# Optimization experiments

Measured on AMD Instinct MI355X. Metric: run time of the kernel, lower is better.

Reference implementation:

```python
import jax, jax.numpy as jnp
import numpy as np

OUT_FEATURES = 16384
IN_FEATURES = 4096


def setup_inputs() -> dict:
    key = jax.random.key(0)
    k1, k2, k3, k4 = jax.random.split(key, 4)
    # activations [B, S, in]
    x = jax.random.normal(k1, (4, 2048, IN_FEATURES), dtype=jnp.float32)
    # packed int4 weights: two nibbles per uint8, total out*in values (even, no pad)
    n_packed = OUT_FEATURES * IN_FEATURES // 2
    weight_packed = jax.random.randint(k2, (n_packed,), 0, 256, dtype=jnp.int32).astype(jnp.uint8)
    # per-row dequant scale [out, 1], positive like abs-max/7
    scale = jax.random.uniform(k3, (OUT_FEATURES, 1), dtype=jnp.float32, minval=1e-3, maxval=0.05)
    bias = jax.random.normal(k4, (OUT_FEATURES,), dtype=jnp.float32) * 0.01
    return {"x": x, "weight_packed": weight_packed, "scale": scale, "bias": bias}


def reference(x, weight_packed, scale, bias):
    # unpack: even positions = low nibble, odd positions = high nibble
    low = (weight_packed & 15).astype(jnp.int8)
    high = ((weight_packed >> 4) & 15).astype(jnp.int8)
    q = jnp.stack([low, high], axis=-1).reshape(-1)  # interleave -> [out*in]
    # sign-extend 4-bit two's complement: values >7 map to negative
    q = jnp.where(q > 7, q - 16, q)
    # dequantize with per-row scale -> [out, in]
    w = q.reshape(OUT_FEATURES, IN_FEATURES).astype(jnp.float32) * scale
    # F.linear: y = x @ w.T + bias
    return jnp.einsum('bsi,oi->bso', x, w) + bias
```

## Files before the change

### kernel.cpp

```cpp
#include <hip/hip_runtime.h>
#include <hip/hip_bf16.h>
#include <stdint.h>

typedef short short8 __attribute__((ext_vector_type(8)));
typedef float floatx4 __attribute__((ext_vector_type(4)));

static constexpr int KTOT = 4096;
static constexpr int NTOT = 16384;
static constexpr int MTOT = 8192;

#define GLOAD_LDS16(g, l)                                              \
  __builtin_amdgcn_global_load_lds(                                    \
      (const __attribute__((address_space(1))) void*)(g),              \
      (__attribute__((address_space(3))) void*)(l), 16, 0, 0)

__device__ __forceinline__ uint32_t pack2_bf16_rne(float lo, float hi) {
  uint32_t a = __builtin_bit_cast(uint32_t, lo);
  uint32_t b = __builtin_bit_cast(uint32_t, hi);
  a += 0x7FFFu + ((a >> 16) & 1u);
  b += 0x7FFFu + ((b >> 16) & 1u);
  return __builtin_amdgcn_perm(b, a, 0x07060302u);
}


__global__ __launch_bounds__(256) void cvt_x_kernel(
    const float* __restrict__ X, ushort* __restrict__ Xb) {
  const size_t i = (size_t)blockIdx.x * 256 + threadIdx.x;
  const float4 a = *reinterpret_cast<const float4*>(X + i * 8);
  const float4 b = *reinterpret_cast<const float4*>(X + i * 8 + 4);
  uint4 o;
  o.x = pack2_bf16_rne(a.x, a.y);
  o.y = pack2_bf16_rne(a.z, a.w);
  o.z = pack2_bf16_rne(b.x, b.y);
  o.w = pack2_bf16_rne(b.z, b.w);
  *reinterpret_cast<uint4*>(Xb + i * 8) = o;
}

__global__ __launch_bounds__(256) void cvt_w_kernel(
    const uint32_t* __restrict__ Wp, ushort* __restrict__ Wb) {
  const size_t i = (size_t)blockIdx.x * 256 + threadIdx.x;
  const uint4 w = *reinterpret_cast<const uint4*>(Wp + i * 4);
  const uint32_t wd[4] = {w.x, w.y, w.z, w.w};
  uint4 o;
  uint32_t* op = reinterpret_cast<uint32_t*>(&o);
  #pragma unroll
  for (int p = 0; p < 4; ++p) {
    int v0 = ((int)(wd[p] << 28)) >> 28;
    int v1 = ((int)(wd[p] << 24)) >> 28;
    uint32_t f0 = __builtin_bit_cast(uint32_t, (float)v0);
    uint32_t f1 = __builtin_bit_cast(uint32_t, (float)v1);
    op[p] = __builtin_amdgcn_perm(f1, f0, 0x07060302u);
  }
  *reinterpret_cast<uint4*>(Wb + i * 8) = o;
}


static constexpr int BM = 256, BN = 256, BK = 32;
static constexpr int NT = KTOT / BK;

__global__ __launch_bounds__(512, 2) void gemm_bf16_256_kernel(
    const ushort* __restrict__ Xb,
    const ushort* __restrict__ Wb,
    const float* __restrict__ scale,
    const float* __restrict__ bias,
    float* __restrict__ Y)
{
  __shared__ ushort As[4 * 8192];
  __shared__ ushort Bs[4 * 8192];

  const int t    = threadIdx.x;
  const int lane = t & 63;
  const int wv   = t >> 6;
  const int wr   = wv >> 2;
  const int wcn  = wv & 3;

  const int wg  = blockIdx.x;
  const int xcd = wg & 7;
  const int s   = wg >> 3;
  const int bm0 = (xcd * 4 + (s & 3)) * BM;
  const int bn0 = (s >> 2) * BN;

  const int srow = wv * 16 + (lane >> 2);
  const int scol = 8 * ((lane & 3) ^ ((lane >> 2) & 3) ^ (lane >> 4));
  const ushort* agA = Xb + (size_t)(bm0 + srow) * KTOT + scol;
  const ushort* agB = Wb + (size_t)(bn0 + srow) * KTOT + scol;
  const size_t rowstep = (size_t)128 * KTOT;
  ushort* aldsw = As + wv * 512;
  ushort* bldsw = Bs + wv * 512;

  const int rcol = 8 * ((lane >> 4) ^ (lane & 3) ^ ((lane >> 2) & 3));
  const ushort* Abase = As + (wr * 128 + (lane & 15)) * 32 + rcol;
  const ushort* Bbase = Bs + (wcn * 64 + (lane & 15)) * 32 + rcol;

  floatx4 acc[8][4];
  #pragma unroll
  for (int m = 0; m < 8; ++m)
    #pragma unroll
    for (int n = 0; n < 4; ++n)
      acc[m][n] = (floatx4){0.f, 0.f, 0.f, 0.f};

  #pragma unroll
  for (int pt = 0; pt < 3; ++pt) {
    const size_t kof = (size_t)pt * BK;
    GLOAD_LDS16(agA + kof,           aldsw + pt * 8192);
    GLOAD_LDS16(agA + kof + rowstep, aldsw + pt * 8192 + 4096);
    GLOAD_LDS16(agB + kof,           bldsw + pt * 8192);
    GLOAD_LDS16(agB + kof + rowstep, bldsw + pt * 8192 + 4096);
  }
  asm volatile("s_waitcnt vmcnt(8)\ns_barrier" ::: "memory");

  for (int kt = 0; kt < NT; ++kt) {
    const int c  = kt & 3;
    const ushort* Ab = Abase + c * 8192;
    const ushort* Bb = Bbase + c * 8192;
    const int st = kt + 3;
    const bool do_stage = (st < NT);
    const int sb = st & 3;
    const size_t kof = (size_t)st * BK;

    short8 bf[4], af0[4], af1[4];
    #pragma unroll
    for (int n = 0; n < 4; ++n)
      bf[n] = *reinterpret_cast<const short8*>(Bb + n * 512);
    #pragma unroll
    for (int m = 0; m < 4; ++m)
      af0[m] = *reinterpret_cast<const short8*>(Ab + m * 512);
    #pragma unroll
    for (int m = 0; m < 4; ++m)
      af1[m] = *reinterpret_cast<const short8*>(Ab + (m + 4) * 512);

    if (do_stage) {
      GLOAD_LDS16(agA + kof,           aldsw + sb * 8192);
      GLOAD_LDS16(agA + kof + rowstep, aldsw + sb * 8192 + 4096);
      GLOAD_LDS16(agB + kof,           bldsw + sb * 8192);
      GLOAD_LDS16(agB + kof + rowstep, bldsw + sb * 8192 + 4096);
    }

    __builtin_amdgcn_s_setprio(1);
    #pragma unroll
    for (int m = 0; m < 4; ++m)
      #pragma unroll
      for (int n = 0; n < 4; ++n)
        acc[m][n] = __builtin_amdgcn_mfma_f32_16x16x32_bf16(af0[m], bf[n], acc[m][n], 0, 0, 0);
    #pragma unroll
    for (int m = 0; m < 4; ++m)
      #pragma unroll
      for (int n = 0; n < 4; ++n)
        acc[m + 4][n] = __builtin_amdgcn_mfma_f32_16x16x32_bf16(af1[m], bf[n], acc[m + 4][n], 0, 0, 0);
    __builtin_amdgcn_s_setprio(0);

    if (kt + 1 < NT) {
      if (kt + 4 <= NT)      { asm volatile("s_waitcnt vmcnt(8)\ns_barrier" ::: "memory"); }
      else if (kt + 3 <= NT) { asm volatile("s_waitcnt vmcnt(4)\ns_barrier" ::: "memory"); }
      else                   { asm volatile("s_waitcnt vmcnt(0)\ns_barrier" ::: "memory"); }
    }
  }

  const int crow = (lane >> 4) * 4;
  const int ccol = lane & 15;
  #pragma unroll
  for (int n = 0; n < 4; ++n) {
    const int col  = bn0 + wcn * 64 + n * 16 + ccol;
    const float sc = scale[col];
    const float bz = bias[col];
    #pragma unroll
    for (int m = 0; m < 8; ++m) {
      const int row0 = bm0 + wr * 128 + m * 16 + crow;
      float* yp = Y + (size_t)row0 * NTOT + col;
      #pragma unroll
      for (int r = 0; r < 4; ++r)
        yp[(size_t)r * NTOT] = acc[m][n][r] * sc + bz;
    }
  }
}


static constexpr int FBM = 128, FBN = 128, FBK = 64;
static constexpr int LDSS = 72;
static constexpr int FNSTEP = KTOT / FBK;

__global__ __launch_bounds__(256) void int4_linear_fused_kernel(
    const float* __restrict__ X,
    const uint32_t* __restrict__ Wp,
    const float* __restrict__ scale,
    const float* __restrict__ bias,
    float* __restrict__ Y)
{
  __shared__ ushort As[FBM * LDSS];
  __shared__ ushort Bs[FBN * LDSS];

  const int t    = threadIdx.x;
  const int lane = t & 63;
  const int wv   = t >> 6;
  const int wr   = wv >> 1;
  const int wc   = wv & 1;
  const int bm0 = blockIdx.y * FBM;
  const int bn0 = blockIdx.x * FBN;
  const int srow = t >> 1;
  const int sh   = t & 1;

  const float*    ag = X  + (size_t)(bm0 + srow) * KTOT + sh * 32;
  const uint32_t* bg = Wp + (size_t)(bn0 + srow) * (KTOT / 2) + sh * 16;

  float4 areg[8];
  uint4  breg[4];
  #pragma unroll
  for (int j = 0; j < 8; ++j) areg[j] = *reinterpret_cast<const float4*>(ag + j * 4);
  #pragma unroll
  for (int j = 0; j < 4; ++j) breg[j] = *reinterpret_cast<const uint4*>(bg + j * 4);

  floatx4 acc[4][4];
  #pragma unroll
  for (int m = 0; m < 4; ++m)
    #pragma unroll
    for (int n = 0; n < 4; ++n)
      acc[m][n] = (floatx4){0.f, 0.f, 0.f, 0.f};

  ushort* adst = &As[srow * LDSS + sh * 32];
  ushort* bdst = &Bs[srow * LDSS + sh * 32];

  for (int ks = 0; ks < FNSTEP; ++ks) {
    {
      uint32_t ab[16];
      #pragma unroll
      for (int j = 0; j < 8; ++j) {
        uint32_t u0 = __builtin_bit_cast(uint32_t, areg[j].x) + 0x8000u;
        uint32_t u1 = __builtin_bit_cast(uint32_t, areg[j].y) + 0x8000u;
        uint32_t u2 = __builtin_bit_cast(uint32_t, areg[j].z) + 0x8000u;
        uint32_t u3 = __builtin_bit_cast(uint32_t, areg[j].w) + 0x8000u;
        ab[2*j]   = __builtin_amdgcn_perm(u1, u0, 0x07060302u);
        ab[2*j+1] = __builtin_amdgcn_perm(u3, u2, 0x07060302u);
      }
      uint32_t bb[16];
      #pragma unroll
      for (int j = 0; j < 4; ++j) {
        const uint32_t wq[4] = {breg[j].x, breg[j].y, breg[j].z, breg[j].w};
        #pragma unroll
        for (int p = 0; p < 4; ++p) {
          const uint32_t w = wq[p];
          int v0 = ((int)(w << 28)) >> 28;
          int v1 = ((int)(w << 24)) >> 28;
          uint32_t f0 = __builtin_bit_cast(uint32_t, (float)v0);
          uint32_t f1 = __builtin_bit_cast(uint32_t, (float)v1);
          bb[j*4 + p] = __builtin_amdgcn_perm(f1, f0, 0x07060302u);
        }
      }
      #pragma unroll
      for (int j = 0; j < 4; ++j) {
        *reinterpret_cast<uint4*>(adst + j * 8) = *reinterpret_cast<const uint4*>(&ab[j*4]);
        *reinterpret_cast<uint4*>(bdst + j * 8) = *reinterpret_cast<const uint4*>(&bb[j*4]);
      }
    }
    __syncthreads();

    if (ks + 1 < FNSTEP) {
      const float*    ap = ag + (ks + 1) * FBK;
      const uint32_t* bp = bg + (ks + 1) * (FBK / 2);
      #pragma unroll
      for (int j = 0; j < 8; ++j) areg[j] = *reinterpret_cast<const float4*>(ap + j * 4);
      #pragma unroll
      for (int j = 0; j < 4; ++j) breg[j] = *reinterpret_cast<const uint4*>(bp + j * 4);
    }

    #pragma unroll
    for (int kk = 0; kk < 2; ++kk) {
      const int ko = kk * 32 + (lane >> 4) * 8;
      short8 af[4], bf[4];
      #pragma unroll
      for (int m = 0; m < 4; ++m)
        af[m] = *reinterpret_cast<const short8*>(&As[(wr*64 + m*16 + (lane & 15)) * LDSS + ko]);
      #pragma unroll
      for (int n = 0; n < 4; ++n)
        bf[n] = *reinterpret_cast<const short8*>(&Bs[(wc*64 + n*16 + (lane & 15)) * LDSS + ko]);
      #pragma unroll
      for (int m = 0; m < 4; ++m)
        #pragma unroll
        for (int n = 0; n < 4; ++n)
          acc[m][n] = __builtin_amdgcn_mfma_f32_16x16x32_bf16(af[m], bf[n], acc[m][n], 0, 0, 0);
    }
    __syncthreads();
  }

  const int crow = (lane >> 4) * 4;
  const int ccol = lane & 15;
  #pragma unroll
  for (int n = 0; n < 4; ++n) {
    const int col  = bn0 + wc * 64 + n * 16 + ccol;
    const float s  = scale[col];
    const float bz = bias[col];
    #pragma unroll
    for (int m = 0; m < 4; ++m) {
      const int row0 = bm0 + wr * 64 + m * 16 + crow;
      float* yp = Y + (size_t)row0 * NTOT + col;
      #pragma unroll
      for (int r = 0; r < 4; ++r)
        yp[(size_t)r * NTOT] = acc[m][n][r] * s + bz;
    }
  }
}


extern "C" void kernel_launch(void* const* d_in, const int* in_sizes, int n_in,
                              void* d_out, int out_size, void* d_ws, size_t ws_size,
                              hipStream_t stream) {
  (void)in_sizes; (void)n_in; (void)out_size;
  const float*    X     = (const float*)d_in[0];
  const uint32_t* Wp    = (const uint32_t*)d_in[1];
  const float*    scale = (const float*)d_in[2];
  const float*    bias  = (const float*)d_in[3];
  float*          Y     = (float*)d_out;

  const size_t xb_bytes = (size_t)MTOT * KTOT * 2;
  const size_t wb_bytes = (size_t)NTOT * KTOT * 2;
  if (ws_size >= xb_bytes + wb_bytes) {
    ushort* Xb = (ushort*)d_ws;
    ushort* Wb = (ushort*)((char*)d_ws + xb_bytes);
    cvt_x_kernel<<<(MTOT * KTOT) / (8 * 256), 256, 0, stream>>>(X, Xb);
    cvt_w_kernel<<<(NTOT * KTOT / 2) / (4 * 256), 256, 0, stream>>>(Wp, Wb);
    gemm_bf16_256_kernel<<<(MTOT / BM) * (NTOT / BN), 512, 0, stream>>>(Xb, Wb, scale, bias, Y);
  } else {
    dim3 grid(NTOT / FBN, MTOT / FBM);
    int4_linear_fused_kernel<<<grid, 256, 0, stream>>>(X, Wp, scale, bias, Y);
  }
}
```

Baseline: 1.182 ms.

## Double-buffer LDS fragments in registers across a 2x unrolled K loop

Unrolls the main K loop by two and keeps two register sets of A/B fragments. The fragments for the next k-tile are read from LDS before the MFMA cluster of the current tile runs, so LDS read latency overlaps matrix math. Wait counts and staging are adjusted so two tiles are resident before compute starts, and the barrier is shifted accordingly. This roughly doubles fragment register usage, which could pressure VGPRs under the 2-blocks-per-CU launch bound.

```diff
diff --git a/kernel.cpp b/kernel.cpp
--- a/kernel.cpp
+++ b/kernel.cpp
@@ -58,6 +58,49 @@
 static constexpr int BM = 256, BN = 256, BK = 32;
 static constexpr int NT = KTOT / BK;
 
+#define READ_FRAGS(AF0, AF1, BF, buf)                                   \
+  {                                                                     \
+    const ushort* Ab_ = Abase + (buf) * 8192;                           \
+    const ushort* Bb_ = Bbase + (buf) * 8192;                           \
+    _Pragma("unroll")                                                   \
+    for (int n = 0; n < 4; ++n)                                         \
+      BF[n] = *reinterpret_cast<const short8*>(Bb_ + n * 512);          \
+    _Pragma("unroll")                                                   \
+    for (int m = 0; m < 4; ++m)                                         \
+      AF0[m] = *reinterpret_cast<const short8*>(Ab_ + m * 512);         \
+    _Pragma("unroll")                                                   \
+    for (int m = 0; m < 4; ++m)                                         \
+      AF1[m] = *reinterpret_cast<const short8*>(Ab_ + (m + 4) * 512);   \
+  }
+
+#define STAGE(st_)                                                      \
+  if ((st_) < NT) {                                                     \
+    const int sb_ = (st_) & 3;                                          \
+    const size_t kof_ = (size_t)(st_) * BK;                             \
+    GLOAD_LDS16(agA + kof_,           aldsw + sb_ * 8192);              \
+    GLOAD_LDS16(agA + kof_ + rowstep, aldsw + sb_ * 8192 + 4096);      \
+    GLOAD_LDS16(agB + kof_,           bldsw + sb_ * 8192);              \
+    GLOAD_LDS16(agB + kof_ + rowstep, bldsw + sb_ * 8192 + 4096);      \
+  }
+
+#define MFMA_CLUSTER(AF0, AF1, BF)                                      \
+  __builtin_amdgcn_s_setprio(1);                                       \
+  _Pragma("unroll")                                                     \
+  for (int m = 0; m < 4; ++m)                                           \
+    _Pragma("unroll")                                                   \
+    for (int n = 0; n < 4; ++n)                                         \
+      acc[m][n] = __builtin_amdgcn_mfma_f32_16x16x32_bf16(AF0[m], BF[n], acc[m][n], 0, 0, 0); \
+  _Pragma("unroll")                                                     \
+  for (int m = 0; m < 4; ++m)                                           \
+    _Pragma("unroll")                                                   \
+    for (int n = 0; n < 4; ++n)                                         \
+      acc[m + 4][n] = __builtin_amdgcn_mfma_f32_16x16x32_bf16(AF1[m], BF[n], acc[m + 4][n], 0, 0, 0); \
+  __builtin_amdgcn_s_setprio(0);
+
+#define BOUNDARY(k_)                                                    \
+  if ((k_) + 3 < NT) { asm volatile("s_waitcnt vmcnt(4)\ns_barrier" ::: "memory"); } \
+  else               { asm volatile("s_waitcnt vmcnt(0)\ns_barrier" ::: "memory"); }
+
 __global__ __launch_bounds__(512, 2) void gemm_bf16_256_kernel(
     const ushort* __restrict__ Xb,
     const ushort* __restrict__ Wb,
@@ -107,53 +150,22 @@
     GLOAD_LDS16(agB + kof,           bldsw + pt * 8192);
     GLOAD_LDS16(agB + kof + rowstep, bldsw + pt * 8192 + 4096);
   }
-  asm volatile("s_waitcnt vmcnt(8)\ns_barrier" ::: "memory");
-
-  for (int kt = 0; kt < NT; ++kt) {
-    const int c  = kt & 3;
-    const ushort* Ab = Abase + c * 8192;
-    const ushort* Bb = Bbase + c * 8192;
-    const int st = kt + 3;
-    const bool do_stage = (st < NT);
-    const int sb = st & 3;
-    const size_t kof = (size_t)st * BK;
-
-    short8 bf[4], af0[4], af1[4];
-    #pragma unroll
-    for (int n = 0; n < 4; ++n)
-      bf[n] = *reinterpret_cast<const short8*>(Bb + n * 512);
-    #pragma unroll
-    for (int m = 0; m < 4; ++m)
-      af0[m] = *reinterpret_cast<const short8*>(Ab + m * 512);
-    #pragma unroll
-    for (int m = 0; m < 4; ++m)
-      af1[m] = *reinterpret_cast<const short8*>(Ab + (m + 4) * 512);
-
-    if (do_stage) {
-      GLOAD_LDS16(agA + kof,           aldsw + sb * 8192);
-      GLOAD_LDS16(agA + kof + rowstep, aldsw + sb * 8192 + 4096);
-      GLOAD_LDS16(agB + kof,           bldsw + sb * 8192);
-      GLOAD_LDS16(agB + kof + rowstep, bldsw + sb * 8192 + 4096);
-    }
-
-    __builtin_amdgcn_s_setprio(1);
-    #pragma unroll
-    for (int m = 0; m < 4; ++m)
-      #pragma unroll
-      for (int n = 0; n < 4; ++n)
-        acc[m][n] = __builtin_amdgcn_mfma_f32_16x16x32_bf16(af0[m], bf[n], acc[m][n], 0, 0, 0);
-    #pragma unroll
-    for (int m = 0; m < 4; ++m)
-      #pragma unroll
-      for (int n = 0; n < 4; ++n)
-        acc[m + 4][n] = __builtin_amdgcn_mfma_f32_16x16x32_bf16(af1[m], bf[n], acc[m + 4][n], 0, 0, 0);
-    __builtin_amdgcn_s_setprio(0);
-
-    if (kt + 1 < NT) {
-      if (kt + 4 <= NT)      { asm volatile("s_waitcnt vmcnt(8)\ns_barrier" ::: "memory"); }
-      else if (kt + 3 <= NT) { asm volatile("s_waitcnt vmcnt(4)\ns_barrier" ::: "memory"); }
-      else                   { asm volatile("s_waitcnt vmcnt(0)\ns_barrier" ::: "memory"); }
-    }
+  asm volatile("s_waitcnt vmcnt(4)\ns_barrier" ::: "memory");
+
+  short8 a0A[4], a1A[4], bA[4];
+  short8 a0B[4], a1B[4], bB[4];
+  READ_FRAGS(a0A, a1A, bA, 0);
+
+  for (int kt = 0; kt < NT; kt += 2) {
+    READ_FRAGS(a0B, a1B, bB, (kt + 1) & 3);
+    STAGE(kt + 3);
+    MFMA_CLUSTER(a0A, a1A, bA);
+    BOUNDARY(kt);
+
+    if (kt + 2 < NT) { READ_FRAGS(a0A, a1A, bA, (kt + 2) & 3); }
+    STAGE(kt + 4);
+    MFMA_CLUSTER(a0B, a1B, bB);
+    if (kt + 2 < NT) { BOUNDARY(kt + 1); }
   }
 
   const int crow = (lane >> 4) * 4;
```

New measurement: 1.105 ms. 6.5% less time.

## Restructure bf16 GEMM main loop into double-buffered BK=64 with four-phase MFMA/load interleave

Applied to the files above, without the earlier changes.

Changes the 256x256 bf16 GEMM from a 4-stage BK=32 ring to a 2-buffer BK=64 scheme. Each k-tile is split into four quadrant phases, each loading A/B fragments from LDS, issuing a slice of next-tile global->LDS loads, then running MFMAs, with barriers between phases. The aim is finer interleaving of loads and MFMAs and fewer loop iterations. In exchange it adds more barriers per tile and shortens prefetch depth to one tile, with a new XOR swizzle for the 64-wide rows.

```diff
diff --git a/kernel.cpp b/kernel.cpp
--- a/kernel.cpp
+++ b/kernel.cpp
@@ -55,8 +55,27 @@
 }
 
 
-static constexpr int BM = 256, BN = 256, BK = 32;
+static constexpr int BM = 256, BN = 256, BK = 64;
 static constexpr int NT = KTOT / BK;
+
+#define BAR_MEM()  asm volatile("s_barrier" ::: "memory")
+#define LGKM0()                                                        \
+  { asm volatile("s_waitcnt lgkmcnt(0)" ::: "memory");                 \
+    __builtin_amdgcn_sched_barrier(0); }
+
+#define MFMA_Q(MB, NB)                                                 \
+  __builtin_amdgcn_s_setprio(1);                                       \
+  _Pragma("unroll")                                                    \
+  for (int m = 0; m < 4; ++m) {                                        \
+    _Pragma("unroll")                                                  \
+    for (int n = 0; n < 2; ++n) {                                      \
+      acc[(MB)+m][(NB)+n] = __builtin_amdgcn_mfma_f32_16x16x32_bf16(   \
+          aK0[m], bK0[n], acc[(MB)+m][(NB)+n], 0, 0, 0);               \
+      acc[(MB)+m][(NB)+n] = __builtin_amdgcn_mfma_f32_16x16x32_bf16(   \
+          aK1[m], bK1[n], acc[(MB)+m][(NB)+n], 0, 0, 0);               \
+    }                                                                  \
+  }                                                                    \
+  __builtin_amdgcn_s_setprio(0);
 
 __global__ __launch_bounds__(512, 2) void gemm_bf16_256_kernel(
     const ushort* __restrict__ Xb,
@@ -65,8 +84,8 @@
     const float* __restrict__ bias,
     float* __restrict__ Y)
 {
-  __shared__ ushort As[4 * 8192];
-  __shared__ ushort Bs[4 * 8192];
+  __shared__ ushort As[2 * 16384];
+  __shared__ ushort Bs[2 * 16384];
 
   const int t    = threadIdx.x;
   const int lane = t & 63;
@@ -80,17 +99,19 @@
   const int bm0 = (xcd * 4 + (s & 3)) * BM;
   const int bn0 = (s >> 2) * BN;
 
-  const int srow = wv * 16 + (lane >> 2);
-  const int scol = 8 * ((lane & 3) ^ ((lane >> 2) & 3) ^ (lane >> 4));
-  const ushort* agA = Xb + (size_t)(bm0 + srow) * KTOT + scol;
-  const ushort* agB = Wb + (size_t)(bn0 + srow) * KTOT + scol;
-  const size_t rowstep = (size_t)128 * KTOT;
-  ushort* aldsw = As + wv * 512;
-  ushort* bldsw = Bs + wv * 512;
-
-  const int rcol = 8 * ((lane >> 4) ^ (lane & 3) ^ ((lane >> 2) & 3));
-  const ushort* Abase = As + (wr * 128 + (lane & 15)) * 32 + rcol;
-  const ushort* Bbase = Bs + (wcn * 64 + (lane & 15)) * 32 + rcol;
+  const int trow = t >> 3;
+  const int scol = 8 * ((t & 7) ^ (trow & 7));
+  const ushort* agA = Xb + (size_t)(bm0 + trow) * KTOT + scol;
+  const ushort* agB = Wb + (size_t)(bn0 + trow) * KTOT + scol;
+  const int ldst = wv * 512;
+
+  const int p   = lane >> 4;
+  const int l7  = lane & 7;
+  const int l15 = lane & 15;
+  const int co0 = 8 * (p ^ l7);
+  const int co1 = 8 * ((4 | p) ^ l7);
+  const int abase = wr * 8192 + l15 * 64;
+  const int bbase = (wcn >> 1) * 8192 + (wcn & 1) * 4096 + l15 * 64;
 
   floatx4 acc[8][4];
   #pragma unroll
@@ -100,60 +121,79 @@
       acc[m][n] = (floatx4){0.f, 0.f, 0.f, 0.f};
 
   #pragma unroll
-  for (int pt = 0; pt < 3; ++pt) {
-    const size_t kof = (size_t)pt * BK;
-    GLOAD_LDS16(agA + kof,           aldsw + pt * 8192);
-    GLOAD_LDS16(agA + kof + rowstep, aldsw + pt * 8192 + 4096);
-    GLOAD_LDS16(agB + kof,           bldsw + pt * 8192);
-    GLOAD_LDS16(agB + kof + rowstep, bldsw + pt * 8192 + 4096);
-  }
-  asm volatile("s_waitcnt vmcnt(8)\ns_barrier" ::: "memory");
+  for (int h = 0; h < 2; ++h)
+    #pragma unroll
+    for (int j = 0; j < 2; ++j) {
+      GLOAD_LDS16(agA + (size_t)(h * 128 + j * 64) * KTOT, As + h * 8192 + j * 4096 + ldst);
+      GLOAD_LDS16(agB + (size_t)(h * 128 + j * 64) * KTOT, Bs + h * 8192 + j * 4096 + ldst);
+    }
+  asm volatile("s_waitcnt vmcnt(0)\ns_barrier" ::: "memory");
+
+  short8 aK0[4], aK1[4], bK0[2], bK1[2];
 
   for (int kt = 0; kt < NT; ++kt) {
-    const int c  = kt & 3;
-    const ushort* Ab = Abase + c * 8192;
-    const ushort* Bb = Bbase + c * 8192;
-    const int st = kt + 3;
-    const bool do_stage = (st < NT);
-    const int sb = st & 3;
-    const size_t kof = (size_t)st * BK;
-
-    short8 bf[4], af0[4], af1[4];
-    #pragma unroll
-    for (int n = 0; n < 4; ++n)
-      bf[n] = *reinterpret_cast<const short8*>(Bb + n * 512);
-    #pragma unroll
-    for (int m = 0; m < 4; ++m)
-      af0[m] = *reinterpret_cast<const short8*>(Ab + m * 512);
-    #pragma unroll
-    for (int m = 0; m < 4; ++m)
-      af1[m] = *reinterpret_cast<const short8*>(Ab + (m + 4) * 512);
-
-    if (do_stage) {
-      GLOAD_LDS16(agA + kof,           aldsw + sb * 8192);
-      GLOAD_LDS16(agA + kof + rowstep, aldsw + sb * 8192 + 4096);
-      GLOAD_LDS16(agB + kof,           bldsw + sb * 8192);
-      GLOAD_LDS16(agB + kof + rowstep, bldsw + sb * 8192 + 4096);
-    }
-
-    __builtin_amdgcn_s_setprio(1);
-    #pragma unroll
-    for (int m = 0; m < 4; ++m)
-      #pragma unroll
-      for (int n = 0; n < 4; ++n)
-        acc[m][n] = __builtin_amdgcn_mfma_f32_16x16x32_bf16(af0[m], bf[n], acc[m][n], 0, 0, 0);
-    #pragma unroll
-    for (int m = 0; m < 4; ++m)
-      #pragma unroll
-      for (int n = 0; n < 4; ++n)
-        acc[m + 4][n] = __builtin_amdgcn_mfma_f32_16x16x32_bf16(af1[m], bf[n], acc[m + 4][n], 0, 0, 0);
-    __builtin_amdgcn_s_setprio(0);
-
-    if (kt + 1 < NT) {
-      if (kt + 4 <= NT)      { asm volatile("s_waitcnt vmcnt(8)\ns_barrier" ::: "memory"); }
-      else if (kt + 3 <= NT) { asm volatile("s_waitcnt vmcnt(4)\ns_barrier" ::: "memory"); }
-      else                   { asm volatile("s_waitcnt vmcnt(0)\ns_barrier" ::: "memory"); }
-    }
+    const int bufo = (kt & 1) << 14;
+    const int sbo  = ((kt + 1) & 1) << 14;
+    const size_t koff = (size_t)(kt + 1) * BK;
+    const bool st = (kt + 1) < NT;
+    const ushort* Abuf = As + bufo;
+    const ushort* Bbuf = Bs + bufo;
+
+    #pragma unroll
+    for (int m = 0; m < 4; ++m) {
+      aK0[m] = *reinterpret_cast<const short8*>(Abuf + abase + m * 1024 + co0);
+      aK1[m] = *reinterpret_cast<const short8*>(Abuf + abase + m * 1024 + co1);
+    }
+    #pragma unroll
+    for (int n = 0; n < 2; ++n) {
+      bK0[n] = *reinterpret_cast<const short8*>(Bbuf + bbase + n * 1024 + co0);
+      bK1[n] = *reinterpret_cast<const short8*>(Bbuf + bbase + n * 1024 + co1);
+    }
+    if (st) {
+      GLOAD_LDS16(agA + koff,                        As + sbo + ldst);
+      GLOAD_LDS16(agA + koff + (size_t)64 * KTOT,    As + sbo + 4096 + ldst);
+    }
+    BAR_MEM(); LGKM0();
+    MFMA_Q(0, 0);
+    BAR_MEM();
+
+    #pragma unroll
+    for (int m = 0; m < 4; ++m) {
+      aK0[m] = *reinterpret_cast<const short8*>(Abuf + abase + (m + 4) * 1024 + co0);
+      aK1[m] = *reinterpret_cast<const short8*>(Abuf + abase + (m + 4) * 1024 + co1);
+    }
+    if (st) {
+      GLOAD_LDS16(agA + koff + (size_t)128 * KTOT,   As + sbo + 8192 + ldst);
+      GLOAD_LDS16(agA + koff + (size_t)192 * KTOT,   As + sbo + 8192 + 4096 + ldst);
+    }
+    BAR_MEM(); LGKM0();
+    MFMA_Q(4, 0);
+    BAR_MEM();
+
+    #pragma unroll
+    for (int n = 0; n < 2; ++n) {
+      bK0[n] = *reinterpret_cast<const short8*>(Bbuf + bbase + (n + 2) * 1024 + co0);
+      bK1[n] = *reinterpret_cast<const short8*>(Bbuf + bbase + (n + 2) * 1024 + co1);
+    }
+    if (st) {
+      GLOAD_LDS16(agB + koff,                        Bs + sbo + ldst);
+      GLOAD_LDS16(agB + koff + (size_t)64 * KTOT,    Bs + sbo + 4096 + ldst);
+      GLOAD_LDS16(agB + koff + (size_t)128 * KTOT,   Bs + sbo + 8192 + ldst);
+      GLOAD_LDS16(agB + koff + (size_t)192 * KTOT,   Bs + sbo + 8192 + 4096 + ldst);
+    }
+    BAR_MEM(); LGKM0();
+    MFMA_Q(4, 2);
+    BAR_MEM();
+
+    #pragma unroll
+    for (int m = 0; m < 4; ++m) {
+      aK0[m] = *reinterpret_cast<const short8*>(Abuf + abase + m * 1024 + co0);
+      aK1[m] = *reinterpret_cast<const short8*>(Abuf + abase + m * 1024 + co1);
+    }
+    BAR_MEM(); LGKM0();
+    MFMA_Q(0, 2);
+    if (st) { asm volatile("s_waitcnt vmcnt(0)\ns_barrier" ::: "memory"); }
+    else    { BAR_MEM(); }
   }
 
   const int crow = (lane >> 4) * 4;
@@ -236,13 +276,13 @@
       for (int j = 0; j < 4; ++j) {
         const uint32_t wq[4] = {breg[j].x, breg[j].y, breg[j].z, breg[j].w};
         #pragma unroll
-        for (int p = 0; p < 4; ++p) {
-          const uint32_t w = wq[p];
+        for (int p2 = 0; p2 < 4; ++p2) {
+          const uint32_t w = wq[p2];
           int v0 = ((int)(w << 28)) >> 28;
           int v1 = ((int)(w << 24)) >> 28;
           uint32_t f0 = __builtin_bit_cast(uint32_t, (float)v0);
           uint32_t f1 = __builtin_bit_cast(uint32_t, (float)v1);
-          bb[j*4 + p] = __builtin_amdgcn_perm(f1, f0, 0x07060302u);
+          bb[j*4 + p2] = __builtin_amdgcn_perm(f1, f0, 0x07060302u);
         }
       }
       #pragma unroll
@@ -286,7 +326,7 @@
   #pragma unroll
   for (int n = 0; n < 4; ++n) {
     const int col  = bn0 + wc * 64 + n * 16 + ccol;
-    const float s  = scale[col];
+    const float sv = scale[col];
     const float bz = bias[col];
     #pragma unroll
     for (int m = 0; m < 4; ++m) {
@@ -294,7 +334,7 @@
       float* yp = Y + (size_t)row0 * NTOT + col;
       #pragma unroll
       for (int r = 0; r < 4; ++r)
-        yp[(size_t)r * NTOT] = acc[m][n][r] * s + bz;
+        yp[(size_t)r * NTOT] = acc[m][n][r] * sv + bz;
     }
   }
 }
```

Result: slower. 1.285 ms (+8.8%).

## Split GEMM k-loop into two barrier-synced phases with new LDS swizzle

Applied to the files above, without the earlier changes.

The main bf16 GEMM loop now runs in two phases. A fragments and the A global-to-LDS stage are issued before the first half of the MFMAs, and the second A half plus the B stage come before the second half. Extra s_barriers and sched_barriers interleave memory traffic with compute, in the style of a ping-pong schedule. The LDS store and read swizzle is also reworked to a new XOR pattern over row pairs, meant to cut bank conflicts. The extra barriers per iteration add synchronisation overhead, and the new swizzle has to match exactly between the stores and the fragment reads.

```diff
diff --git a/kernel.cpp b/kernel.cpp
--- a/kernel.cpp
+++ b/kernel.cpp
@@ -58,6 +58,27 @@
 static constexpr int BM = 256, BN = 256, BK = 32;
 static constexpr int NT = KTOT / BK;
 
+#define STAGE_A2(st_)                                                   \
+  if ((st_) < NT) {                                                     \
+    const int sb_ = (st_) & 3;                                          \
+    const size_t kof_ = (size_t)(st_) * BK;                             \
+    GLOAD_LDS16(agA + kof_,           aldsw + sb_ * 8192);              \
+    GLOAD_LDS16(agA + kof_ + rowstep, aldsw + sb_ * 8192 + 4096);       \
+  }
+
+#define STAGE_B2(st_)                                                   \
+  if ((st_) < NT) {                                                     \
+    const int sb_ = (st_) & 3;                                          \
+    const size_t kof_ = (size_t)(st_) * BK;                             \
+    GLOAD_LDS16(agB + kof_,           bldsw + sb_ * 8192);              \
+    GLOAD_LDS16(agB + kof_ + rowstep, bldsw + sb_ * 8192 + 4096);       \
+  }
+
+#define PH_SYNC()                                                       \
+  { asm volatile("s_barrier" ::: "memory");                             \
+    asm volatile("s_waitcnt lgkmcnt(0)" ::: "memory");                  \
+    __builtin_amdgcn_sched_barrier(0); }
+
 __global__ __launch_bounds__(512, 2) void gemm_bf16_256_kernel(
     const ushort* __restrict__ Xb,
     const ushort* __restrict__ Wb,
@@ -80,17 +101,21 @@
   const int bm0 = (xcd * 4 + (s & 3)) * BM;
   const int bn0 = (s >> 2) * BN;
 
-  const int srow = wv * 16 + (lane >> 2);
-  const int scol = 8 * ((lane & 3) ^ ((lane >> 2) & 3) ^ (lane >> 4));
+  const int clg  = (t & 7) ^ ((t >> 3) & 7);
+  const int srow = ((t >> 3) << 1) | (clg >> 2);
+  const int scol = (clg & 3) * 8;
   const ushort* agA = Xb + (size_t)(bm0 + srow) * KTOT + scol;
   const ushort* agB = Wb + (size_t)(bn0 + srow) * KTOT + scol;
   const size_t rowstep = (size_t)128 * KTOT;
   ushort* aldsw = As + wv * 512;
   ushort* bldsw = Bs + wv * 512;
 
-  const int rcol = 8 * ((lane >> 4) ^ (lane & 3) ^ ((lane >> 2) & 3));
-  const ushort* Abase = As + (wr * 128 + (lane & 15)) * 32 + rcol;
-  const ushort* Bbase = Bs + (wcn * 64 + (lane & 15)) * 32 + rcol;
+  const int p    = lane >> 4;
+  const int l15  = lane & 15;
+  const int cph  = (((l15 & 1) << 2) | p) ^ ((l15 >> 1) & 7);
+  const int laneoff = (l15 >> 1) * 64 + cph * 8;
+  const int abase = wr * 4096;
+  const int bbase = wcn * 2048;
 
   floatx4 acc[8][4];
   #pragma unroll
@@ -109,51 +134,46 @@
   }
   asm volatile("s_waitcnt vmcnt(8)\ns_barrier" ::: "memory");
 
+  short8 aF0[4], aF1[4], bF[4];
+
   for (int kt = 0; kt < NT; ++kt) {
-    const int c  = kt & 3;
-    const ushort* Ab = Abase + c * 8192;
-    const ushort* Bb = Bbase + c * 8192;
+    const ushort* Ab_ = As + (kt & 3) * 8192 + abase + laneoff;
+    const ushort* Bb_ = Bs + (kt & 3) * 8192 + bbase + laneoff;
     const int st = kt + 3;
-    const bool do_stage = (st < NT);
-    const int sb = st & 3;
-    const size_t kof = (size_t)st * BK;
-
-    short8 bf[4], af0[4], af1[4];
+
     #pragma unroll
     for (int n = 0; n < 4; ++n)
-      bf[n] = *reinterpret_cast<const short8*>(Bb + n * 512);
+      bF[n] = *reinterpret_cast<const short8*>(Bb_ + n * 512);
     #pragma unroll
     for (int m = 0; m < 4; ++m)
-      af0[m] = *reinterpret_cast<const short8*>(Ab + m * 512);
+      aF0[m] = *reinterpret_cast<const short8*>(Ab_ + m * 512);
+    STAGE_A2(st);
+    PH_SYNC();
+    __builtin_amdgcn_s_setprio(1);
     #pragma unroll
     for (int m = 0; m < 4; ++m)
-      af1[m] = *reinterpret_cast<const short8*>(Ab + (m + 4) * 512);
-
-    if (do_stage) {
-      GLOAD_LDS16(agA + kof,           aldsw + sb * 8192);
-      GLOAD_LDS16(agA + kof + rowstep, aldsw + sb * 8192 + 4096);
-      GLOAD_LDS16(agB + kof,           bldsw + sb * 8192);
-      GLOAD_LDS16(agB + kof + rowstep, bldsw + sb * 8192 + 4096);
-    }
-
+      #pragma unroll
+      for (int n = 0; n < 4; ++n)
+        acc[m][n] = __builtin_amdgcn_mfma_f32_16x16x32_bf16(aF0[m], bF[n], acc[m][n], 0, 0, 0);
+    __builtin_amdgcn_s_setprio(0);
+    asm volatile("s_barrier" ::: "memory");
+
+    #pragma unroll
+    for (int m = 0; m < 4; ++m)
+      aF1[m] = *reinterpret_cast<const short8*>(Ab_ + (m + 4) * 512);
+    STAGE_B2(st);
+    PH_SYNC();
     __builtin_amdgcn_s_setprio(1);
     #pragma unroll
     for (int m = 0; m < 4; ++m)
       #pragma unroll
       for (int n = 0; n < 4; ++n)
-        acc[m][n] = __builtin_amdgcn_mfma_f32_16x16x32_bf16(af0[m], bf[n], acc[m][n], 0, 0, 0);
-    #pragma unroll
-    for (int m = 0; m < 4; ++m)
-      #pragma unroll
-      for (int n = 0; n < 4; ++n)
-        acc[m + 4][n] = __builtin_amdgcn_mfma_f32_16x16x32_bf16(af1[m], bf[n], acc[m + 4][n], 0, 0, 0);
+        acc[m + 4][n] = __builtin_amdgcn_mfma_f32_16x16x32_bf16(aF1[m], bF[n], acc[m + 4][n], 0, 0, 0);
     __builtin_amdgcn_s_setprio(0);
 
-    if (kt + 1 < NT) {
-      if (kt + 4 <= NT)      { asm volatile("s_waitcnt vmcnt(8)\ns_barrier" ::: "memory"); }
-      else if (kt + 3 <= NT) { asm volatile("s_waitcnt vmcnt(4)\ns_barrier" ::: "memory"); }
-      else                   { asm volatile("s_waitcnt vmcnt(0)\ns_barrier" ::: "memory"); }
-    }
+    if (kt + 4 <= NT)      { asm volatile("s_waitcnt vmcnt(8)\ns_barrier" ::: "memory"); }
+    else if (kt + 3 <= NT) { asm volatile("s_waitcnt vmcnt(4)\ns_barrier" ::: "memory"); }
+    else if (kt + 2 <= NT) { asm volatile("s_waitcnt vmcnt(0)\ns_barrier" ::: "memory"); }
   }
 
   const int crow = (lane >> 4) * 4;
@@ -236,13 +256,13 @@
       for (int j = 0; j < 4; ++j) {
         const uint32_t wq[4] = {breg[j].x, breg[j].y, breg[j].z, breg[j].w};
         #pragma unroll
-        for (int p = 0; p < 4; ++p) {
-          const uint32_t w = wq[p];
+        for (int p2 = 0; p2 < 4; ++p2) {
+          const uint32_t w = wq[p2];
           int v0 = ((int)(w << 28)) >> 28;
           int v1 = ((int)(w << 24)) >> 28;
           uint32_t f0 = __builtin_bit_cast(uint32_t, (float)v0);
           uint32_t f1 = __builtin_bit_cast(uint32_t, (float)v1);
-          bb[j*4 + p] = __builtin_amdgcn_perm(f1, f0, 0x07060302u);
+          bb[j*4 + p2] = __builtin_amdgcn_perm(f1, f0, 0x07060302u);
         }
       }
       #pragma unroll
@@ -286,7 +306,7 @@
   #pragma unroll
   for (int n = 0; n < 4; ++n) {
     const int col  = bn0 + wc * 64 + n * 16 + ccol;
-    const float s  = scale[col];
+    const float sv = scale[col];
     const float bz = bias[col];
     #pragma unroll
     for (int m = 0; m < 4; ++m) {
@@ -294,7 +314,7 @@
       float* yp = Y + (size_t)row0 * NTOT + col;
       #pragma unroll
       for (int r = 0; r < 4; ++r)
-        yp[(size_t)r * NTOT] = acc[m][n][r] * s + bz;
+        yp[(size_t)r * NTOT] = acc[m][n][r] * sv + bz;
     }
   }
 }
```

Result: slower. 1.232 ms (+4.2%).
